# Optimization experiments

Measured on AMD Instinct MI355X. Metric: run time of the kernel, lower is better.

## Reference

```python
import jax, jax.numpy as jnp
import numpy as np

B, D, H = 524288, 64, 19  # batch, input_size, hidden_size


def setup_inputs() -> dict:
    key = jax.random.key(0)
    ks = jax.random.split(key, 4)
    x = jax.random.normal(ks[0], (B, D), dtype=jnp.float32)
    # nn.Linear params (stored as [out, in] like torch)
    Wi = jax.random.normal(ks[1], (H, D), dtype=jnp.float32) / np.sqrt(D).astype(np.float32)
    bi = jnp.zeros((H,), jnp.float32)
    Wr = jax.random.normal(ks[2], (H, H), dtype=jnp.float32) / np.sqrt(H).astype(np.float32)
    Wo = jax.random.normal(ks[3], (H, H), dtype=jnp.float32) / np.sqrt(H).astype(np.float32)
    bo = jnp.zeros((H,), jnp.float32)
    tau = jnp.full((H,), 0.5, jnp.float32)        # nn.Parameter(ones*0.5)
    tau_adapt = jnp.full((H,), 0.1, jnp.float32)  # nn.Parameter(ones*0.1)
    return {"x": x, "Wi": Wi, "bi": bi, "Wr": Wr, "Wo": Wo, "bo": bo,
            "tau": tau, "tau_adapt": tau_adapt, "steps": 10}


def reference(x, Wi, bi, Wr, Wo, bo, tau, tau_adapt, steps):
    dt = 0.01
    # scalar urgency over the whole input, clamped from below
    urgency = jnp.maximum(jnp.abs(x).mean(), 0.01)
    tau_dyn = jnp.clip(tau * (1.0 - tau_adapt) + tau_adapt / urgency, 0.01, 10.0)  # [H]
    mapped = x @ Wi.T + bi  # [B, H], computed once outside the loop
    h0 = jnp.zeros((x.shape[0], tau.shape[0]), x.dtype)

    def step(h, _):
        act = jnp.tanh(mapped + h @ Wr.T)
        h = h + dt * ((-h + act) / tau_dyn)
        return h, None

    h, _ = jax.lax.scan(step, h0, None, length=steps)
    return (h @ Wo.T + bo, h)
```

## Files before the change

kernel.cpp:

```cpp
#include <hip/hip_runtime.h>

#define NB 524288
#define ND 64
#define NH 19
#define NP 10
#define NBLK 2048

typedef float v2f __attribute__((ext_vector_type(2)));

__device__ __forceinline__ v2f splat2(float x) { return (v2f){x, x}; }
__device__ __forceinline__ v2f fma2(v2f a, v2f b, v2f c) {
    return __builtin_elementwise_fma(a, b, c);
}
__device__ __forceinline__ float rfl(float v) {
    union { float f; int i; } a; a.f = v;
    a.i = __builtin_amdgcn_readfirstlane(a.i);
    return a.f;
}

__device__ __forceinline__ v2f tanh2(v2f x) {
    const float c = 2.8853900817779268f;
    float ex = __builtin_amdgcn_exp2f(x.x * c);
    float ey = __builtin_amdgcn_exp2f(x.y * c);
    v2f r = {__builtin_amdgcn_rcpf(ex + 1.f), __builtin_amdgcn_rcpf(ey + 1.f)};
    return fma2(splat2(-2.f), r, splat2(1.f));
}

#define WAVE_LDS_FENCE()                                      \
    do {                                                      \
        asm volatile("s_waitcnt lgkmcnt(0)" ::: "memory");    \
        __builtin_amdgcn_sched_barrier(0);                    \
    } while (0)

extern "C" __global__ void __launch_bounds__(64)
ltc_setup(const float* __restrict__ Wi, const float* __restrict__ bi,
          const float* __restrict__ Wr, const float* __restrict__ Wo,
          const float* __restrict__ bo,
          float2* __restrict__ Wi2, float2* __restrict__ bi2,
          float2* __restrict__ Wr2, float2* __restrict__ Wo2,
          float2* __restrict__ bo2)
{
    for (int i = threadIdx.x; i < NH * NP; i += 64) {
        int k = i / NP, t = i % NP;
        float rx = Wr[(2 * t) * NH + k];
        float ry = (2 * t + 1 < NH) ? Wr[(2 * t + 1) * NH + k] : 0.f;
        Wr2[i] = make_float2(rx, ry);
        float ox = Wo[(2 * t) * NH + k];
        float oy = (2 * t + 1 < NH) ? Wo[(2 * t + 1) * NH + k] : 0.f;
        Wo2[i] = make_float2(ox, oy);
    }
    for (int i = threadIdx.x; i < ND * NP; i += 64) {
        int col = i / NP, t = i % NP;
        float ax = Wi[(2 * t) * ND + col];
        float ay = (2 * t + 1 < NH) ? Wi[(2 * t + 1) * ND + col] : 0.f;
        Wi2[i] = make_float2(ax, ay);
    }
    if (threadIdx.x < NP) {
        int t = threadIdx.x;
        bo2[t] = make_float2(bo[2 * t], (2 * t + 1 < NH) ? bo[2 * t + 1] : 0.f);
        bi2[t] = make_float2(bi[2 * t], (2 * t + 1 < NH) ? bi[2 * t + 1] : 0.f);
    }
}

extern "C" __global__ void __launch_bounds__(256)
ltc_absum(const float* __restrict__ x, float* __restrict__ partials)
{
    __shared__ float red[4];
    const int t = threadIdx.x;
    const float4* xg = (const float4*)x + (size_t)blockIdx.x * 4096;
    float s = 0.f;
#pragma unroll
    for (int i = 0; i < 16; ++i) {
        const float4 v = xg[i * 256 + t];
        s += fabsf(v.x) + fabsf(v.y) + fabsf(v.z) + fabsf(v.w);
    }
#pragma unroll
    for (int off = 32; off > 0; off >>= 1) s += __shfl_down(s, off, 64);
    if ((t & 63) == 0) red[t >> 6] = s;
    __syncthreads();
    if (t == 0) partials[blockIdx.x] = red[0] + red[1] + red[2] + red[3];
}

extern "C" __global__ void __launch_bounds__(256)
ltc_fused(const float* __restrict__ x, const float* __restrict__ partials,
          const v2f* __restrict__ Wi2, const v2f* __restrict__ bi2,
          const v2f* __restrict__ Wr2, const v2f* __restrict__ Wo2,
          const v2f* __restrict__ bo2, const float* __restrict__ tau,
          const float* __restrict__ ta, const int* __restrict__ steps_p,
          float* __restrict__ out)
{
    __shared__ float lds[4 * 64 * 34];
    __shared__ v2f wrl[NH * NP];
    __shared__ float red[4];
    const int t = threadIdx.x;
    const int l = t & 63, w = t >> 6;
    const int rowbase = blockIdx.x * 256;

    if (t < NH * NP) wrl[t] = Wr2[t];

    float ps = 0.f;
#pragma unroll
    for (int i = 0; i < NBLK / 256; ++i) ps += partials[t + 256 * i];
#pragma unroll
    for (int off = 32; off > 0; off >>= 1) ps += __shfl_down(ps, off, 64);
    if ((t & 63) == 0) red[t >> 6] = ps;
    __syncthreads();
    const float total = red[0] + red[1] + red[2] + red[3];
    const float u = rfl(fmaxf(total * (1.f / ((float)NB * (float)ND)), 0.01f));
    const float inv_u = 1.f / u;

    v2f m2[NP];
#pragma unroll
    for (int j = 0; j < NP; ++j) m2[j] = bi2[j];
    {
        float* tw = lds + w * (64 * 34);
        const float4* xg = (const float4*)x + (size_t)(rowbase + w * 64) * 16;
#pragma unroll
        for (int c = 0; c < 2; ++c) {
#pragma unroll
            for (int i = 0; i < 8; ++i) {
                const int flat = i * 64 + l, row = flat >> 3, cq = flat & 7;
                const float4 v = xg[row * 16 + c * 8 + cq];
                *(float2*)&tw[row * 34 + cq * 4]     = make_float2(v.x, v.y);
                *(float2*)&tw[row * 34 + cq * 4 + 2] = make_float2(v.z, v.w);
            }
            WAVE_LDS_FENCE();
#pragma unroll
            for (int q = 0; q < 16; ++q) {
                const float2 v = *(const float2*)&tw[l * 34 + 2 * q];
                const int col = c * 32 + 2 * q;
                const v2f vx = splat2(v.x), vy = splat2(v.y);
                const v2f* wc0 = Wi2 + (size_t)col * NP;
                const v2f* wc1 = Wi2 + (size_t)(col + 1) * NP;
#pragma unroll
                for (int j = 0; j < NP; ++j) m2[j] = fma2(vx, wc0[j], m2[j]);
#pragma unroll
                for (int j = 0; j < NP; ++j) m2[j] = fma2(vy, wc1[j], m2[j]);
            }
            WAVE_LDS_FENCE();
        }
    }

    v2f rr2[NP];
#pragma unroll
    for (int j = 0; j < NP; ++j) {
        int j0 = 2 * j, j1 = (2 * j + 1 < NH) ? 2 * j + 1 : 2 * j;
        float t0 = fminf(10.f, fmaxf(0.01f, tau[j0] * (1.f - ta[j0]) + ta[j0] * inv_u));
        float t1 = fminf(10.f, fmaxf(0.01f, tau[j1] * (1.f - ta[j1]) + ta[j1] * inv_u));
        rr2[j] = (v2f){0.01f / t0, 0.01f / t1};
    }

    v2f h2[NP];
#pragma unroll
    for (int j = 0; j < NP; ++j) h2[j] = splat2(0.f);

    const int steps = *steps_p;
    const v2f* wr = wrl;
    for (int s = 0; s < steps; ++s) {
        v2f p2[NP];
        {
            const v2f hb = splat2(h2[0].x);
#pragma unroll
            for (int j = 0; j < NP; ++j) p2[j] = fma2(hb, wr[j], m2[j]);
        }
#pragma unroll
        for (int k = 1; k < NH; ++k) {
            const float hk = (k & 1) ? h2[k >> 1].y : h2[k >> 1].x;
            const v2f hb = splat2(hk);
            const v2f* wrow = wr + k * NP;
#pragma unroll
            for (int j = 0; j < NP; ++j) p2[j] = fma2(hb, wrow[j], p2[j]);
        }
#pragma unroll
        for (int j = 0; j < NP; ++j) p2[j] = tanh2(p2[j]);
#pragma unroll
        for (int j = 0; j < NP; ++j) h2[j] = fma2(rr2[j], p2[j] - h2[j], h2[j]);
    }

    const v2f* wo = Wo2;
    v2f o2[NP];
    {
        const v2f hb = splat2(h2[0].x);
#pragma unroll
        for (int j = 0; j < NP; ++j) o2[j] = fma2(hb, wo[j], bo2[j]);
    }
#pragma unroll
    for (int k = 1; k < NH; ++k) {
        const float hk = (k & 1) ? h2[k >> 1].y : h2[k >> 1].x;
        const v2f hb = splat2(hk);
        const v2f* worow = wo + k * NP;
#pragma unroll
        for (int j = 0; j < NP; ++j) o2[j] = fma2(hb, worow[j], o2[j]);
    }
    float* st = lds;
    __syncthreads();
#pragma unroll
    for (int j = 0; j < NH; ++j)
        st[t * NH + j] = (j & 1) ? o2[j >> 1].y : o2[j >> 1].x;
    __syncthreads();
    {
        const float4* s4 = (const float4*)st;
        float4* o4 = (float4*)(out + (size_t)blockIdx.x * 256 * NH);
#pragma unroll
        for (int i = 0; i < 4; ++i) o4[t + i * 256] = s4[t + i * 256];
        if (t + 1024 < 1216) o4[t + 1024] = s4[t + 1024];
    }
    __syncthreads();
#pragma unroll
    for (int j = 0; j < NH; ++j)
        st[t * NH + j] = (j & 1) ? h2[j >> 1].y : h2[j >> 1].x;
    __syncthreads();
    {
        const float4* s4 = (const float4*)st;
        float4* o4 = (float4*)(out + (size_t)NB * NH + (size_t)blockIdx.x * 256 * NH);
#pragma unroll
        for (int i = 0; i < 4; ++i) o4[t + i * 256] = s4[t + i * 256];
        if (t + 1024 < 1216) o4[t + 1024] = s4[t + 1024];
    }
}

extern "C" void kernel_launch(void* const* d_in, const int* in_sizes, int n_in,
                              void* d_out, int out_size, void* d_ws, size_t ws_size,
                              hipStream_t stream)
{
    const float* x   = (const float*)d_in[0];
    const float* Wi  = (const float*)d_in[1];
    const float* bi  = (const float*)d_in[2];
    const float* Wr  = (const float*)d_in[3];
    const float* Wo  = (const float*)d_in[4];
    const float* bo  = (const float*)d_in[5];
    const float* tau = (const float*)d_in[6];
    const float* ta  = (const float*)d_in[7];
    const int* steps = (const int*)d_in[8];
    float* out = (float*)d_out;

    float*  partials = (float*)d_ws;
    float2* Wr2 = (float2*)((char*)d_ws + 8192);
    float2* Wo2 = (float2*)((char*)d_ws + 9728);
    float2* bo2 = (float2*)((char*)d_ws + 11264);
    float2* bi2 = (float2*)((char*)d_ws + 11360);
    float2* Wi2 = (float2*)((char*)d_ws + 11456);

    ltc_setup<<<1, 64, 0, stream>>>(Wi, bi, Wr, Wo, bo, Wi2, bi2, Wr2, Wo2, bo2);
    ltc_absum<<<NBLK, 256, 0, stream>>>(x, partials);
    ltc_fused<<<NBLK, 256, 0, stream>>>(x, partials, (const v2f*)Wi2,
                                        (const v2f*)bi2, (const v2f*)Wr2,
                                        (const v2f*)Wo2, (const v2f*)bo2,
                                        tau, ta, steps, out);
}
```

Measured before the change: 406.3 us.

## Process two rows per thread to reuse recurrent weight loads across rows

Each thread now handles two batch rows, so the fused kernel launches half as many blocks and each recurrent and output weight load feeds two independent FMA chains. Wr is read from global memory (uniform, scalar-cacheable) instead of an LDS copy, and the wave-local LDS fences become block-wide barriers. The kernel is marked for at most 3 waves per EU, giving more registers for the doubled state. This trades occupancy and parallelism for more instruction-level parallelism and fewer weight loads per row.

```diff
diff --git a/kernel.cpp b/kernel.cpp
--- a/kernel.cpp
+++ b/kernel.cpp
@@ -4,7 +4,8 @@
 #define ND 64
 #define NH 19
 #define NP 10
-#define NBLK 2048
+#define NBLK_ABS 2048
+#define NBLK_F 1024
 
 typedef float v2f __attribute__((ext_vector_type(2)));
 
@@ -25,12 +26,6 @@
     v2f r = {__builtin_amdgcn_rcpf(ex + 1.f), __builtin_amdgcn_rcpf(ey + 1.f)};
     return fma2(splat2(-2.f), r, splat2(1.f));
 }
-
-#define WAVE_LDS_FENCE()                                      \
-    do {                                                      \
-        asm volatile("s_waitcnt lgkmcnt(0)" ::: "memory");    \
-        __builtin_amdgcn_sched_barrier(0);                    \
-    } while (0)
 
 extern "C" __global__ void __launch_bounds__(64)
 ltc_setup(const float* __restrict__ Wi, const float* __restrict__ bi,
@@ -81,7 +76,9 @@
     if (t == 0) partials[blockIdx.x] = red[0] + red[1] + red[2] + red[3];
 }
 
-extern "C" __global__ void __launch_bounds__(256)
+extern "C" __global__ void
+__launch_bounds__(256)
+__attribute__((amdgpu_waves_per_eu(1, 3)))
 ltc_fused(const float* __restrict__ x, const float* __restrict__ partials,
           const v2f* __restrict__ Wi2, const v2f* __restrict__ bi2,
           const v2f* __restrict__ Wr2, const v2f* __restrict__ Wo2,
@@ -90,17 +87,14 @@
           float* __restrict__ out)
 {
     __shared__ float lds[4 * 64 * 34];
-    __shared__ v2f wrl[NH * NP];
     __shared__ float red[4];
     const int t = threadIdx.x;
     const int l = t & 63, w = t >> 6;
-    const int rowbase = blockIdx.x * 256;
-
-    if (t < NH * NP) wrl[t] = Wr2[t];
+    const int rowbase = blockIdx.x * 512;
 
     float ps = 0.f;
 #pragma unroll
-    for (int i = 0; i < NBLK / 256; ++i) ps += partials[t + 256 * i];
+    for (int i = 0; i < NBLK_ABS / 256; ++i) ps += partials[t + 256 * i];
 #pragma unroll
     for (int off = 32; off > 0; off >>= 1) ps += __shfl_down(ps, off, 64);
     if ((t & 63) == 0) red[t >> 6] = ps;
@@ -109,35 +103,40 @@
     const float u = rfl(fmaxf(total * (1.f / ((float)NB * (float)ND)), 0.01f));
     const float inv_u = 1.f / u;
 
-    v2f m2[NP];
-#pragma unroll
-    for (int j = 0; j < NP; ++j) m2[j] = bi2[j];
+    v2f m2a[NP], m2b[NP];
+#pragma unroll
+    for (int j = 0; j < NP; ++j) { m2a[j] = bi2[j]; m2b[j] = bi2[j]; }
     {
         float* tw = lds + w * (64 * 34);
-        const float4* xg = (const float4*)x + (size_t)(rowbase + w * 64) * 16;
-#pragma unroll
-        for (int c = 0; c < 2; ++c) {
-#pragma unroll
-            for (int i = 0; i < 8; ++i) {
-                const int flat = i * 64 + l, row = flat >> 3, cq = flat & 7;
-                const float4 v = xg[row * 16 + c * 8 + cq];
-                *(float2*)&tw[row * 34 + cq * 4]     = make_float2(v.x, v.y);
-                *(float2*)&tw[row * 34 + cq * 4 + 2] = make_float2(v.z, v.w);
+#pragma unroll 1
+        for (int pass = 0; pass < 2; ++pass) {
+            v2f* m2 = pass ? m2b : m2a;
+            const float4* xg = (const float4*)x +
+                               (size_t)(rowbase + pass * 256 + w * 64) * 16;
+#pragma unroll
+            for (int c = 0; c < 2; ++c) {
+#pragma unroll
+                for (int i = 0; i < 8; ++i) {
+                    const int flat = i * 64 + l, row = flat >> 3, cq = flat & 7;
+                    const float4 v = xg[row * 16 + c * 8 + cq];
+                    *(float2*)&tw[row * 34 + cq * 4]     = make_float2(v.x, v.y);
+                    *(float2*)&tw[row * 34 + cq * 4 + 2] = make_float2(v.z, v.w);
+                }
+                __syncthreads();
+#pragma unroll
+                for (int q = 0; q < 16; ++q) {
+                    const float2 v = *(const float2*)&tw[l * 34 + 2 * q];
+                    const int col = c * 32 + 2 * q;
+                    const v2f vx = splat2(v.x), vy = splat2(v.y);
+                    const v2f* wc0 = Wi2 + (size_t)col * NP;
+                    const v2f* wc1 = Wi2 + (size_t)(col + 1) * NP;
+#pragma unroll
+                    for (int j = 0; j < NP; ++j) m2[j] = fma2(vx, wc0[j], m2[j]);
+#pragma unroll
+                    for (int j = 0; j < NP; ++j) m2[j] = fma2(vy, wc1[j], m2[j]);
+                }
+                __syncthreads();
             }
-            WAVE_LDS_FENCE();
-#pragma unroll
-            for (int q = 0; q < 16; ++q) {
-                const float2 v = *(const float2*)&tw[l * 34 + 2 * q];
-                const int col = c * 32 + 2 * q;
-                const v2f vx = splat2(v.x), vy = splat2(v.y);
-                const v2f* wc0 = Wi2 + (size_t)col * NP;
-                const v2f* wc1 = Wi2 + (size_t)(col + 1) * NP;
-#pragma unroll
-                for (int j = 0; j < NP; ++j) m2[j] = fma2(vx, wc0[j], m2[j]);
-#pragma unroll
-                for (int j = 0; j < NP; ++j) m2[j] = fma2(vy, wc1[j], m2[j]);
-            }
-            WAVE_LDS_FENCE();
         }
     }
 
@@ -150,73 +149,94 @@
         rr2[j] = (v2f){0.01f / t0, 0.01f / t1};
     }
 
-    v2f h2[NP];
-#pragma unroll
-    for (int j = 0; j < NP; ++j) h2[j] = splat2(0.f);
+    v2f h2a[NP], h2b[NP];
+#pragma unroll
+    for (int j = 0; j < NP; ++j) { h2a[j] = splat2(0.f); h2b[j] = splat2(0.f); }
 
     const int steps = *steps_p;
-    const v2f* wr = wrl;
+    const v2f* wr = Wr2;
+#pragma unroll 1
     for (int s = 0; s < steps; ++s) {
-        v2f p2[NP];
+        v2f p2a[NP], p2b[NP];
         {
-            const v2f hb = splat2(h2[0].x);
-#pragma unroll
-            for (int j = 0; j < NP; ++j) p2[j] = fma2(hb, wr[j], m2[j]);
+            const v2f ha = splat2(h2a[0].x), hb = splat2(h2b[0].x);
+#pragma unroll
+            for (int j = 0; j < NP; ++j) {
+                const v2f wv = wr[j];
+                p2a[j] = fma2(ha, wv, m2a[j]);
+                p2b[j] = fma2(hb, wv, m2b[j]);
+            }
         }
 #pragma unroll
         for (int k = 1; k < NH; ++k) {
-            const float hk = (k & 1) ? h2[k >> 1].y : h2[k >> 1].x;
-            const v2f hb = splat2(hk);
+            const float hka = (k & 1) ? h2a[k >> 1].y : h2a[k >> 1].x;
+            const float hkb = (k & 1) ? h2b[k >> 1].y : h2b[k >> 1].x;
+            const v2f ha = splat2(hka), hb = splat2(hkb);
             const v2f* wrow = wr + k * NP;
 #pragma unroll
-            for (int j = 0; j < NP; ++j) p2[j] = fma2(hb, wrow[j], p2[j]);
-        }
-#pragma unroll
-        for (int j = 0; j < NP; ++j) p2[j] = tanh2(p2[j]);
-#pragma unroll
-        for (int j = 0; j < NP; ++j) h2[j] = fma2(rr2[j], p2[j] - h2[j], h2[j]);
+            for (int j = 0; j < NP; ++j) {
+                const v2f wv = wrow[j];
+                p2a[j] = fma2(ha, wv, p2a[j]);
+                p2b[j] = fma2(hb, wv, p2b[j]);
+            }
+        }
+#pragma unroll
+        for (int j = 0; j < NP; ++j) p2a[j] = tanh2(p2a[j]);
+#pragma unroll
+        for (int j = 0; j < NP; ++j) p2b[j] = tanh2(p2b[j]);
+#pragma unroll
+        for (int j = 0; j < NP; ++j) {
+            h2a[j] = fma2(rr2[j], p2a[j] - h2a[j], h2a[j]);
+            h2b[j] = fma2(rr2[j], p2b[j] - h2b[j], h2b[j]);
+        }
     }
 
     const v2f* wo = Wo2;
-    v2f o2[NP];
+    v2f o2a[NP], o2b[NP];
     {
-        const v2f hb = splat2(h2[0].x);
-#pragma unroll
-        for (int j = 0; j < NP; ++j) o2[j] = fma2(hb, wo[j], bo2[j]);
+        const v2f ha = splat2(h2a[0].x), hb = splat2(h2b[0].x);
+#pragma unroll
+        for (int j = 0; j < NP; ++j) {
+            const v2f wv = wo[j], bb = bo2[j];
+            o2a[j] = fma2(ha, wv, bb);
+            o2b[j] = fma2(hb, wv, bb);
+        }
     }
 #pragma unroll
     for (int k = 1; k < NH; ++k) {
-        const float hk = (k & 1) ? h2[k >> 1].y : h2[k >> 1].x;
-        const v2f hb = splat2(hk);
+        const float hka = (k & 1) ? h2a[k >> 1].y : h2a[k >> 1].x;
+        const float hkb = (k & 1) ? h2b[k >> 1].y : h2b[k >> 1].x;
+        const v2f ha = splat2(hka), hb = splat2(hkb);
         const v2f* worow = wo + k * NP;
 #pragma unroll
-        for (int j = 0; j < NP; ++j) o2[j] = fma2(hb, worow[j], o2[j]);
-    }
+        for (int j = 0; j < NP; ++j) {
+            const v2f wv = worow[j];
+            o2a[j] = fma2(ha, wv, o2a[j]);
+            o2b[j] = fma2(hb, wv, o2b[j]);
+        }
+    }
+
     float* st = lds;
     __syncthreads();
-#pragma unroll
-    for (int j = 0; j < NH; ++j)
-        st[t * NH + j] = (j & 1) ? o2[j >> 1].y : o2[j >> 1].x;
-    __syncthreads();
-    {
-        const float4* s4 = (const float4*)st;
-        float4* o4 = (float4*)(out + (size_t)blockIdx.x * 256 * NH);
-#pragma unroll
-        for (int i = 0; i < 4; ++i) o4[t + i * 256] = s4[t + i * 256];
-        if (t + 1024 < 1216) o4[t + 1024] = s4[t + 1024];
-    }
-    __syncthreads();
-#pragma unroll
-    for (int j = 0; j < NH; ++j)
-        st[t * NH + j] = (j & 1) ? h2[j >> 1].y : h2[j >> 1].x;
-    __syncthreads();
-    {
-        const float4* s4 = (const float4*)st;
-        float4* o4 = (float4*)(out + (size_t)NB * NH + (size_t)blockIdx.x * 256 * NH);
-#pragma unroll
-        for (int i = 0; i < 4; ++i) o4[t + i * 256] = s4[t + i * 256];
-        if (t + 1024 < 1216) o4[t + 1024] = s4[t + 1024];
-    }
+#define STAGE_STORE(arr, dstp)                                              \
+    do {                                                                    \
+        _Pragma("unroll")                                                   \
+        for (int j = 0; j < NH; ++j)                                        \
+            st[t * NH + j] = (j & 1) ? arr[j >> 1].y : arr[j >> 1].x;       \
+        __syncthreads();                                                    \
+        const float4* s4 = (const float4*)st;                               \
+        float4* o4 = (float4*)(dstp);                                       \
+        _Pragma("unroll")                                                   \
+        for (int i = 0; i < 4; ++i) o4[t + i * 256] = s4[t + i * 256];      \
+        if (t + 1024 < 1216) o4[t + 1024] = s4[t + 1024];                   \
+        __syncthreads();                                                    \
+    } while (0)
+
+    STAGE_STORE(o2a, out + (size_t)blockIdx.x * 512 * NH);
+    STAGE_STORE(o2b, out + (size_t)blockIdx.x * 512 * NH + 256 * NH);
+    STAGE_STORE(h2a, out + (size_t)NB * NH + (size_t)blockIdx.x * 512 * NH);
+    STAGE_STORE(h2b, out + (size_t)NB * NH + (size_t)blockIdx.x * 512 * NH + 256 * NH);
+#undef STAGE_STORE
 }
 
 extern "C" void kernel_launch(void* const* d_in, const int* in_sizes, int n_in,
@@ -242,9 +262,9 @@
     float2* Wi2 = (float2*)((char*)d_ws + 11456);
 
     ltc_setup<<<1, 64, 0, stream>>>(Wi, bi, Wr, Wo, bo, Wi2, bi2, Wr2, Wo2, bo2);
-    ltc_absum<<<NBLK, 256, 0, stream>>>(x, partials);
-    ltc_fused<<<NBLK, 256, 0, stream>>>(x, partials, (const v2f*)Wi2,
-                                        (const v2f*)bi2, (const v2f*)Wr2,
-                                        (const v2f*)Wo2, (const v2f*)bo2,
-                                        tau, ta, steps, out);
-}
+    ltc_absum<<<NBLK_ABS, 256, 0, stream>>>(x, partials);
+    ltc_fused<<<NBLK_F, 256, 0, stream>>>(x, partials, (const v2f*)Wi2,
+                                          (const v2f*)bi2, (const v2f*)Wr2,
+                                          (const v2f*)Wo2, (const v2f*)bo2,
+                                          tau, ta, steps, out);
+}
```

Result: faster. 370.3 us (-8.9%).
